# Performance work log

Hardware: AMD Instinct MI355X
Metric: run time of the kernel (lower is better)

The kernel has to match this reference:

```python
import jax, jax.numpy as jnp
import numpy as np

B, S, T = 256, 512, 32  # batch, seq_len, tag_size (includes START=T-2, END=T-1)


def setup_inputs() -> dict:
    key = jax.random.key(0)
    k1, k2, k3, k4 = jax.random.split(key, 4)
    feats = jax.random.normal(k1, (B, S, T), dtype=jnp.float32)
    transitions = jax.random.normal(k2, (T, T), dtype=jnp.float32) * 0.1
    # prefix mask: lengths in [S//2, S] (torch code assumes contiguous valid prefix)
    lengths = jax.random.randint(k3, (B,), S // 2, S + 1)
    mask = jnp.arange(S)[None, :] < lengths[:, None]  # (B,S) bool
    tags = jax.random.randint(k4, (B, S), 0, T - 2).astype(jnp.int32)
    return {"feats": feats, "transitions": transitions, "mask": mask, "tags": tags}


def _nll_loss(feats, transitions, mask, tags):
    Bx, Sx, Tx = feats.shape
    maskf = mask.astype(feats.dtype)
    # ---- forward algorithm (log partition) ----
    # partition initialized from emissions at position 1 (positions 0,1 are special)
    part0 = feats[:, 1, :]  # (B,T)
    f_seq = jnp.swapaxes(feats[:, 2:, :], 0, 1)  # (S-2, B, T)
    m_seq = jnp.swapaxes(mask[:, 2:], 0, 1)      # (S-2, B)

    def fwd_step(partition, inp):
        f_t, m_t = inp
        # cur[b, prev, next] = feats[b,t,next] + transitions[prev,next] + partition[b,prev]
        cur = f_t[:, None, :] + transitions[None, :, :] + partition[:, :, None]
        new = jax.nn.logsumexp(cur, axis=1)  # (B,T)
        # partition frozen where mask==0 (== torch masked_scatter logic)
        return jnp.where(m_t[:, None], new, partition), None

    partition, _ = jax.lax.scan(fwd_step, part0, (f_seq, m_seq))
    forward_score = jnp.sum(jax.nn.logsumexp(partition, axis=1))

    # ---- gold score ----
    tags = jnp.where(tags == -100, 0, tags)
    emis = jnp.take_along_axis(feats, tags[..., None], axis=2)[..., 0]  # (B,S)
    tr = transitions[tags[:, :-1], tags[:, 1:]]  # (B,S-1): transition into pos t (t>=1)
    # transitions only apply for t>=2; tg_energy[0] is zeroed in the torch code
    e = emis + jnp.concatenate([jnp.zeros((Bx, 2), feats.dtype), tr[:, 1:]], axis=1)
    e = e.at[:, 0].set(0.0)
    gold_score = jnp.sum(e * maskf)
    return (forward_score - gold_score) / Bx


def _viterbi(feats, transitions, mask):
    Bx, Sx, Tx = feats.shape
    lengths = mask.astype(jnp.int32).sum(axis=1)
    part0 = feats[:, 1, :]
    f_seq = jnp.swapaxes(feats[:, 2:, :], 0, 1)
    m_seq = jnp.swapaxes(mask[:, 2:], 0, 1)

    def vit_step(partition, inp):
        f_t, m_t = inp
        cur = f_t[:, None, :] + transitions[None, :, :] + partition[:, :, None]
        new = jnp.max(cur, axis=1)
        bp = jnp.argmax(cur, axis=1).astype(jnp.int32)
        bp = jnp.where(m_t[:, None], bp, 0)  # torch masked_fill_(pad, 0)
        # NOTE: viterbi partition is updated UNconditionally in the torch code
        return new, (partition, bp)

    last_part, (hist, bps) = jax.lax.scan(vit_step, part0, (f_seq, m_seq))
    history = jnp.concatenate([hist, last_part[None]], axis=0)  # (S-1,B,T)
    hist_bt = jnp.swapaxes(history, 0, 1)                        # (B,S-1,T)
    idx = jnp.broadcast_to((lengths - 2)[:, None, None], (Bx, 1, Tx))
    last_partition = jnp.take_along_axis(hist_bt, idx, axis=1)[:, 0, :]  # (B,T)
    pointer = jnp.argmax(last_partition, axis=1).astype(jnp.int32)

    def back_step(ptr, bp_t):
        new = jnp.take_along_axis(bp_t, ptr[:, None], axis=1)[:, 0]
        return new, new

    _, ptrs = jax.lax.scan(back_step, pointer, bps, reverse=True)  # (S-2,B)
    # decode_idx[0] is uninitialized in the torch code; we define it as 0
    decode = jnp.concatenate(
        [jnp.zeros((1, Bx), jnp.int32), ptrs, pointer[None, :]], axis=0
    )  # (S,B)
    path_score = jnp.zeros((Bx,), feats.dtype)  # torch returns zeros
    return path_score, decode.T


def reference(feats, transitions, mask, tags):
    loss = _nll_loss(feats, transitions, mask, tags)
    path_score, decode_idx = _viterbi(feats, transitions, mask)
    return loss, path_score, decode_idx
```

## Files before the change

kernel.cpp:

```cpp
#include <hip/hip_runtime.h>
#include <cstdint>
#include <cstddef>
#include <utility>

#define SS 512
#define TT 32
#define NB 256
#define KSTEPS 510
#define PQUADS 128

template <typename F, size_t... Is>
__device__ __forceinline__ void unroll_impl(F&& f, std::index_sequence<Is...>) {
  (f(std::integral_constant<int, (int)Is>{}), ...);
}
template <int N, typename F>
__device__ __forceinline__ void unrollN(F&& f) {
  unroll_impl(f, std::make_index_sequence<N>{});
}

template <int D>
__device__ __forceinline__ float bfly32(float v) {
  return __int_as_float(__builtin_amdgcn_ds_swizzle(__float_as_int(v), (D << 10) | 0x1f));
}
template <int D>
__device__ __forceinline__ int bfly32i(int v) {
  return __builtin_amdgcn_ds_swizzle(v, (D << 10) | 0x1f);
}

__device__ __forceinline__ float max3f(float a, float b, float c) {
  return fmaxf(fmaxf(a, b), c);
}

template <int R>
__device__ __forceinline__ float dpp_rorf(float v) {
  return __int_as_float(__builtin_amdgcn_update_dpp(
      0, __float_as_int(v), 0x120 + R, 0xf, 0xf, true));
}
template <int R>
__device__ __forceinline__ int dpp_rori(int v) {
  return __builtin_amdgcn_update_dpp(0, v, 0x120 + R, 0xf, 0xf, true);
}

__device__ __forceinline__ float combine_max32(float m) {
#if __has_builtin(__builtin_amdgcn_permlane32_swap)
  auto r = __builtin_amdgcn_permlane32_swap(__float_as_uint(m), __float_as_uint(m), false, false);
  return fmaxf(__uint_as_float(r[0]), __uint_as_float(r[1]));
#else
  return fmaxf(m, __shfl_xor(m, 32, 64));
#endif
}
__device__ __forceinline__ float combine_sum32(float m) {
#if __has_builtin(__builtin_amdgcn_permlane32_swap)
  auto r = __builtin_amdgcn_permlane32_swap(__float_as_uint(m), __float_as_uint(m), false, false);
  return __uint_as_float(r[0]) + __uint_as_float(r[1]);
#else
  return m + __shfl_xor(m, 32, 64);
#endif
}
__device__ __forceinline__ float partner16(float v) {
#if __has_builtin(__builtin_amdgcn_permlane16_swap)
  auto r = __builtin_amdgcn_permlane16_swap(__float_as_uint(v), __float_as_uint(v), false, false);
  float a = __uint_as_float(r[0]), b = __uint_as_float(r[1]);
  return (__float_as_uint(a) == __float_as_uint(v)) ? b : a;
#else
  return __shfl_xor(v, 16, 64);
#endif
}

__device__ __forceinline__ int mask_mode(const void* m) {
  int w0 = ((const int*)m)[0];
  if (w0 == 1) return 0;
  if (w0 == 0x3f800000) return 2;
  return 1;
}
__device__ __forceinline__ bool mask_at(const void* m, int idx, int mode) {
  if (mode == 0) return ((const int*)m)[idx] != 0;
  if (mode == 2) return ((const float*)m)[idx] != 0.0f;
  return ((const unsigned char*)m)[idx] != 0;
}

__device__ __forceinline__ int seq_length_lane(const void* mask, int b, int lane, int mode) {
  int cnt = 0;
  for (int s = lane; s < SS; s += 64) cnt += mask_at(mask, b * SS + s, mode) ? 1 : 0;
  for (int d = 1; d < 64; d <<= 1) cnt += __shfl_xor(cnt, d, 64);
  return __builtin_amdgcn_readfirstlane(cnt);
}

__global__ __launch_bounds__(64, 1) void crf_main_kernel(
    const float* __restrict__ feats, const float* __restrict__ trans,
    const void* __restrict__ mask, const int* __restrict__ tags,
    float* __restrict__ pstore, float* __restrict__ ws_fwd,
    float* __restrict__ ws_gold, int* __restrict__ ws_ptr) {
  const int blk = blockIdx.x;
  const int tid = threadIdx.x;
  const int mode = mask_mode(mask);
  const int lane = tid & 63;
  const int l15 = lane & 15;
  const int row = lane >> 4;
  const int heldB = (row == 1 || row == 2) ? 16 : 0;
  const int outB  = (row == 1 || row == 3) ? 16 : 0;
  const int heldtag = l15 + heldB;
  const int outtag  = l15 + outB;
  const bool lower = (lane < 32);

  int src15[16];
  src15[0] = l15;
  unrollN<15>([&](auto RR) { constexpr int r = RR + 1; src15[r] = dpp_rori<r>(l15); });

  if (blk < NB) {
    const int b = blk;
    const int steps = seq_length_lane(mask, b, tid, mode) - 2;
    const float* fb = feats + (size_t)b * (SS * TT) + outtag;

    float E[16];
    unrollN<16>([&](auto RR) {
      constexpr int r = RR;
      E[r] = __expf(trans[(src15[r] + heldB) * TT + outtag]);
    });

    float q = __expf(feats[(size_t)b * (SS * TT) + TT + heldtag]);
    int Eacc = 0;
    float fA = fb[2 * TT], fB = fb[3 * TT], fC = fb[4 * TT];
    float ef = __expf(fA);

    auto fstep = [&](int k, bool resc) {
      int r5 = k + 5; r5 = (r5 < SS) ? r5 : (SS - 1);
      float fD = fb[r5 * TT];
      float efN = __expf(fB);
      float a0 = q * E[0], a1, a2, a3;
      a1 = dpp_rorf<1>(q) * E[1];
      a2 = dpp_rorf<2>(q) * E[2];
      a3 = dpp_rorf<3>(q) * E[3];
      a0 = fmaf(dpp_rorf<4>(q),  E[4],  a0);
      a1 = fmaf(dpp_rorf<5>(q),  E[5],  a1);
      a2 = fmaf(dpp_rorf<6>(q),  E[6],  a2);
      a3 = fmaf(dpp_rorf<7>(q),  E[7],  a3);
      a0 = fmaf(dpp_rorf<8>(q),  E[8],  a0);
      a1 = fmaf(dpp_rorf<9>(q),  E[9],  a1);
      a2 = fmaf(dpp_rorf<10>(q), E[10], a2);
      a3 = fmaf(dpp_rorf<11>(q), E[11], a3);
      a0 = fmaf(dpp_rorf<12>(q), E[12], a0);
      a1 = fmaf(dpp_rorf<13>(q), E[13], a1);
      a2 = fmaf(dpp_rorf<14>(q), E[14], a2);
      a3 = fmaf(dpp_rorf<15>(q), E[15], a3);
      float P = (a0 + a1) + (a2 + a3);
      float val = ef * combine_sum32(P);
      float par = partner16(val);
      float qn = lower ? val : par;
      if (resc) {
        int qb = __builtin_amdgcn_readfirstlane(__float_as_int(qn));
        int e = (qb >> 23) & 0xff;
        Eacc += e - 127;
        qn *= __int_as_float((254 - e) << 23);
      }
      q = qn;
      fA = fB; fB = fC; fC = fD; ef = efN;
    };

    int k = 0;
    for (; k + 4 <= steps; k += 4) {
      fstep(k, false); fstep(k + 1, false); fstep(k + 2, false); fstep(k + 3, true);
    }
    for (; k < steps; ++k) fstep(k, false);

    float s = q;
    unrollN<5>([&](auto D) { constexpr int d = 1 << D; s += bfly32<d>(s); });
    if (tid == 0) ws_fwd[b] = __logf(s) + (float)Eacc * 0.69314718056f;

  } else if (blk < 2 * NB) {
    const int b = blk - NB;
    const int steps = seq_length_lane(mask, b, tid, mode) - 2;
    const float* fb = feats + (size_t)b * (SS * TT) + outtag;
    float* pq = pstore + (size_t)b * (PQUADS * 128) + lane * 4;

    float C[16];
    unrollN<16>([&](auto RR) {
      constexpr int r = RR;
      C[r] = trans[(src15[r] + heldB) * TT + outtag];
    });

    float p = feats[(size_t)b * (SS * TT) + TT + heldtag];
    float fA = fb[2 * TT], fB = fb[3 * TT], fC = fb[4 * TT];
    float h0 = p, h1 = 0.f, h2 = 0.f, h3 = 0.f;

    auto vstep = [&](int k, float& hslot) {
      int r5 = k + 5; r5 = (r5 < SS) ? r5 : (SS - 1);
      float fD = fb[r5 * TT];
      float dd[16];
      unrollN<16>([&](auto RR) { constexpr int r = RR; dd[r] = fA + C[r]; });
      float cur[16];
      cur[0] = p + dd[0];
      cur[1]  = dpp_rorf<1>(p)  + dd[1];
      cur[2]  = dpp_rorf<2>(p)  + dd[2];
      cur[3]  = dpp_rorf<3>(p)  + dd[3];
      cur[4]  = dpp_rorf<4>(p)  + dd[4];
      cur[5]  = dpp_rorf<5>(p)  + dd[5];
      cur[6]  = dpp_rorf<6>(p)  + dd[6];
      cur[7]  = dpp_rorf<7>(p)  + dd[7];
      cur[8]  = dpp_rorf<8>(p)  + dd[8];
      cur[9]  = dpp_rorf<9>(p)  + dd[9];
      cur[10] = dpp_rorf<10>(p) + dd[10];
      cur[11] = dpp_rorf<11>(p) + dd[11];
      cur[12] = dpp_rorf<12>(p) + dd[12];
      cur[13] = dpp_rorf<13>(p) + dd[13];
      cur[14] = dpp_rorf<14>(p) + dd[14];
      cur[15] = dpp_rorf<15>(p) + dd[15];
      float t0 = max3f(cur[0], cur[1], cur[2]);
      float t1 = max3f(cur[3], cur[4], cur[5]);
      float t2 = max3f(cur[6], cur[7], cur[8]);
      float t3 = max3f(cur[9], cur[10], cur[11]);
      float t4 = max3f(cur[12], cur[13], cur[14]);
      float m = fmaxf(max3f(t0, t1, t2), max3f(t3, t4, cur[15]));
      float full = combine_max32(m);
      float par = partner16(full);
      float pw = lower ? full : par;
      p = pw;
      hslot = pw;
      fA = fB; fB = fC; fC = fD;
    };

    auto flush = [&](int quad) {
      if (lane < 32) {
        float4 v; v.x = h0; v.y = h1; v.z = h2; v.w = h3;
        *(float4*)(pq + quad * 128) = v;
      }
    };

    int k = 0;
    for (; k + 4 <= steps; k += 4) {
      vstep(k, h1);
      vstep(k + 1, h2);
      vstep(k + 2, h3);
      flush(k >> 2);
      vstep(k + 3, h0);
    }
    if (k < steps) vstep(k, h1);
    if (k + 1 < steps) vstep(k + 1, h2);
    if (k + 2 < steps) vstep(k + 2, h3);
    flush(k >> 2);

    float v = p;
    int idx = lane & 31;
    unrollN<5>([&](auto D) {
      constexpr int d = 1 << D;
      float vo = bfly32<d>(v);
      int io = bfly32i<d>(idx);
      bool take = (vo > v) || ((vo == v) && (io < idx));
      v = take ? vo : v;
      idx = take ? io : idx;
    });
    if (tid == 0) ws_ptr[b] = idx;

  } else {
    const int b = blk - 2 * NB;
    float acc = 0.0f;
    for (int s = tid; s < SS; s += 64) {
      if (s == 0) continue;
      if (!mask_at(mask, b * SS + s, mode)) continue;
      int tg = tags[b * SS + s];
      if (tg == -100) tg = 0;
      float e = feats[((size_t)b * SS + s) * TT + tg];
      if (s >= 2) {
        int tp = tags[b * SS + s - 1];
        if (tp == -100) tp = 0;
        e += trans[tp * TT + tg];
      }
      acc += e;
    }
    for (int d = 1; d < 64; d <<= 1) acc += __shfl_xor(acc, d, 64);
    if (tid == 0) ws_gold[b] = acc;
  }
}

__global__ __launch_bounds__(512) void crf_backtrace_kernel(
    const float* __restrict__ pstore, const float* __restrict__ feats,
    const float* __restrict__ trans, const void* __restrict__ mask,
    const int* __restrict__ ws_ptr, const float* __restrict__ ws_fwd,
    const float* __restrict__ ws_gold, float* __restrict__ out) {
  __shared__ unsigned char bp[KSTEPS * TT];
  __shared__ unsigned char path[KSTEPS * TT];
  __shared__ __align__(16) float pT[16][4][TT];
  __shared__ int entries[8];

  const int b = blockIdx.x;
  const int tid = threadIdx.x;
  const int mode = mask_mode(mask);
  const int lane = tid & 63;
  float* out_decode = out + 1 + NB;

  const int steps = seq_length_lane(mask, b, lane, mode) - 2;

  if (tid == 0) out[1 + b] = 0.0f;
  if (b == 0 && tid >= 64 && tid < 128) {
    int t = tid - 64;
    float sf = 0.0f, sg = 0.0f;
    for (int r = 0; r < 4; ++r) { sf += ws_fwd[t + 64 * r]; sg += ws_gold[t + 64 * r]; }
    for (int d = 1; d < 64; d <<= 1) { sf += __shfl_xor(sf, d, 64); sg += __shfl_xor(sg, d, 64); }
    if (t == 0) out[0] = (sf - sg) / 256.0f;
  }

  {
    const int jj = tid & 31;
    const int g = tid >> 5;
    float Cc[TT];
    unrollN<TT>([&](auto I) { constexpr int ii = I; Cc[ii] = trans[ii * TT + jj]; });
    const float* pb = pstore + (size_t)b * (PQUADS * 128);
    const float* fbb = feats + (size_t)b * (SS * TT);
    for (int q = g; q < PQUADS; q += 16) {
      float4 V = *(const float4*)(pb + q * 128 + jj * 4);
      pT[g][0][jj] = V.x; pT[g][1][jj] = V.y; pT[g][2][jj] = V.z; pT[g][3][jj] = V.w;
      asm volatile("" ::: "memory");
      unrollN<4>([&](auto R) {
        constexpr int r = R;
        const int k = 4 * q + r;
        if (k < KSTEPS) {
          unsigned char bv = 0;
          if (k < steps) {
            const float4* pr = (const float4*)pT[g][r];
            float4 P0 = pr[0], P1 = pr[1], P2 = pr[2], P3 = pr[3];
            float4 P4 = pr[4], P5 = pr[5], P6 = pr[6], P7 = pr[7];
            float fj = fbb[(k + 2) * TT + jj];
            float cur[TT];
            cur[0]  = (fj + Cc[0])  + P0.x; cur[1]  = (fj + Cc[1])  + P0.y;
            cur[2]  = (fj + Cc[2])  + P0.z; cur[3]  = (fj + Cc[3])  + P0.w;
            cur[4]  = (fj + Cc[4])  + P1.x; cur[5]  = (fj + Cc[5])  + P1.y;
            cur[6]  = (fj + Cc[6])  + P1.z; cur[7]  = (fj + Cc[7])  + P1.w;
            cur[8]  = (fj + Cc[8])  + P2.x; cur[9]  = (fj + Cc[9])  + P2.y;
            cur[10] = (fj + Cc[10]) + P2.z; cur[11] = (fj + Cc[11]) + P2.w;
            cur[12] = (fj + Cc[12]) + P3.x; cur[13] = (fj + Cc[13]) + P3.y;
            cur[14] = (fj + Cc[14]) + P3.z; cur[15] = (fj + Cc[15]) + P3.w;
            cur[16] = (fj + Cc[16]) + P4.x; cur[17] = (fj + Cc[17]) + P4.y;
            cur[18] = (fj + Cc[18]) + P4.z; cur[19] = (fj + Cc[19]) + P4.w;
            cur[20] = (fj + Cc[20]) + P5.x; cur[21] = (fj + Cc[21]) + P5.y;
            cur[22] = (fj + Cc[22]) + P5.z; cur[23] = (fj + Cc[23]) + P5.w;
            cur[24] = (fj + Cc[24]) + P6.x; cur[25] = (fj + Cc[25]) + P6.y;
            cur[26] = (fj + Cc[26]) + P6.z; cur[27] = (fj + Cc[27]) + P6.w;
            cur[28] = (fj + Cc[28]) + P7.x; cur[29] = (fj + Cc[29]) + P7.y;
            cur[30] = (fj + Cc[30]) + P7.z; cur[31] = (fj + Cc[31]) + P7.w;
            float t0 = max3f(cur[0], cur[1], cur[2]);
            float t1 = max3f(cur[3], cur[4], cur[5]);
            float t2 = max3f(cur[6], cur[7], cur[8]);
            float t3 = max3f(cur[9], cur[10], cur[11]);
            float t4 = max3f(cur[12], cur[13], cur[14]);
            float t5 = max3f(cur[15], cur[16], cur[17]);
            float t6 = max3f(cur[18], cur[19], cur[20]);
            float t7 = max3f(cur[21], cur[22], cur[23]);
            float t8 = max3f(cur[24], cur[25], cur[26]);
            float t9 = max3f(cur[27], cur[28], cur[29]);
            float ta = fmaxf(cur[30], cur[31]);
            float vmax = fmaxf(fmaxf(max3f(t0, t1, t2), max3f(t3, t4, t5)),
                               fmaxf(max3f(t6, t7, t8), fmaxf(t9, ta)));
            int bi = 31;
            unrollN<TT>([&](auto I) { constexpr int ii = 31 - I; bi = (cur[ii] == vmax) ? ii : bi; });
            bv = (unsigned char)bi;
          }
          bp[k * TT + jj] = bv;
        }
      });
    }
  }
  __syncthreads();

  const int wave = tid >> 6;
  if (lane < 32) {
    const int lo = wave * 64;
    const int hi = (lo + 64 < KSTEPS) ? (lo + 64) : KSTEPS;
    int ptr = lane;
    for (int k = hi - 1; k >= lo; --k) {
      ptr = bp[k * TT + ptr];
      path[k * TT + lane] = (unsigned char)ptr;
    }
  }
  __syncthreads();

  if (tid == 0) {
    int e = ws_ptr[b];
    for (int c = 7; c >= 0; --c) {
      entries[c] = e;
      e = path[(c * 64) * TT + e];
    }
  }
  __syncthreads();

  const int s = tid;
  int val;
  if (s == 0) val = 0;
  else if (s <= KSTEPS) { int k = s - 1; val = path[k * TT + entries[k >> 6]]; }
  else val = ws_ptr[b];
  out_decode[(size_t)b * SS + s] = (float)val;
}

extern "C" void kernel_launch(void* const* d_in, const int* in_sizes, int n_in,
                              void* d_out, int out_size, void* d_ws, size_t ws_size,
                              hipStream_t stream) {
  const float* feats = (const float*)d_in[0];
  const float* trans = (const float*)d_in[1];
  const void* mask = d_in[2];
  const int* tags = (const int*)d_in[3];
  float* out = (float*)d_out;

  unsigned char* ws = (unsigned char*)d_ws;
  const size_t PST_BYTES = (size_t)NB * PQUADS * 128 * 4;
  float* pstore = (float*)ws;
  float* ws_fwd = (float*)(ws + PST_BYTES);
  float* ws_gold = (float*)(ws + PST_BYTES + 2048);
  int* ws_ptr = (int*)(ws + PST_BYTES + 4096);

  hipLaunchKernelGGL(crf_main_kernel, dim3(3 * NB), dim3(64), 0, stream,
                     feats, trans, mask, tags, pstore, ws_fwd, ws_gold, ws_ptr);
  hipLaunchKernelGGL(crf_backtrace_kernel, dim3(NB), dim3(512), 0, stream,
                     pstore, feats, trans, mask, ws_ptr, ws_fwd, ws_gold, out);
}
```

Before: 103.6 us.

## Transpose feats to tag-major layout so recurrences load float4 rows

Adds a pre-pass kernel that transposes feats from (B,S,T) to (B,T,S) in workspace. The forward and Viterbi recurrences then read four timesteps per lane with one float4 load instead of one strided scalar load per step, which is meant to cut latency-bound memory traffic in the serial loop. The new path is used only when the workspace is large enough, with the old kernel kept as a fallback. It costs an extra launch and a full read and write of feats (about 16 MB each way).

After: 113.5 us. 1.1x slower.

```diff
diff --git a/kernel.cpp b/kernel.cpp
--- a/kernel.cpp
+++ b/kernel.cpp
@@ -86,7 +86,227 @@
   return __builtin_amdgcn_readfirstlane(cnt);
 }
 
-__global__ __launch_bounds__(64, 1) void crf_main_kernel(
+__global__ __launch_bounds__(256) void crf_transpose_kernel(
+    const float* __restrict__ feats, float* __restrict__ ftr) {
+  const int b = blockIdx.x;
+  const int tid = threadIdx.x;
+  __shared__ float tile[TT][72];
+
+  for (int tile0 = 0; tile0 < SS; tile0 += 64) {
+    for (int i = tid; i < 512; i += 256) {
+      int s_local = i >> 3, g = i & 7;
+      float4 v = *(const float4*)(feats + ((size_t)(b * SS + tile0 + s_local)) * TT + 4 * g);
+      tile[4 * g + 0][s_local] = v.x;
+      tile[4 * g + 1][s_local] = v.y;
+      tile[4 * g + 2][s_local] = v.z;
+      tile[4 * g + 3][s_local] = v.w;
+    }
+    __syncthreads();
+    {
+      int t = tid >> 3, sc = tid & 7;
+      float4 a, c;
+      a.x = tile[t][sc * 8 + 0]; a.y = tile[t][sc * 8 + 1];
+      a.z = tile[t][sc * 8 + 2]; a.w = tile[t][sc * 8 + 3];
+      c.x = tile[t][sc * 8 + 4]; c.y = tile[t][sc * 8 + 5];
+      c.z = tile[t][sc * 8 + 6]; c.w = tile[t][sc * 8 + 7];
+      float* dst = ftr + ((size_t)(b * TT + t)) * SS + tile0 + sc * 8;
+      *(float4*)dst = a;
+      *(float4*)(dst + 4) = c;
+    }
+    __syncthreads();
+  }
+}
+
+__global__ __launch_bounds__(64, 1) void crf_main_kernel_t(
+    const float* __restrict__ feats, const float* __restrict__ ftr,
+    const float* __restrict__ trans, const void* __restrict__ mask,
+    const int* __restrict__ tags, float* __restrict__ pstore,
+    float* __restrict__ ws_fwd, float* __restrict__ ws_gold,
+    int* __restrict__ ws_ptr) {
+  const int blk = blockIdx.x;
+  const int tid = threadIdx.x;
+  const int mode = mask_mode(mask);
+  const int lane = tid & 63;
+  const int l15 = lane & 15;
+  const int row = lane >> 4;
+  const int heldB = (row == 1 || row == 2) ? 16 : 0;
+  const int outB  = (row == 1 || row == 3) ? 16 : 0;
+  const int heldtag = l15 + heldB;
+  const int outtag  = l15 + outB;
+  const bool lower = (lane < 32);
+
+  int src15[16];
+  src15[0] = l15;
+  unrollN<15>([&](auto RR) { constexpr int r = RR + 1; src15[r] = dpp_rori<r>(l15); });
+
+  if (blk < NB) {
+    const int b = blk;
+    const int steps = seq_length_lane(mask, b, tid, mode) - 2;
+    const float* fr = ftr + ((size_t)(b * TT + outtag)) * SS;
+
+    float E[16];
+    unrollN<16>([&](auto RR) {
+      constexpr int r = RR;
+      E[r] = __expf(trans[(src15[r] + heldB) * TT + outtag]);
+    });
+
+    float q = __expf(ftr[((size_t)(b * TT + heldtag)) * SS + 1]);
+    int Eacc = 0;
+
+    auto fstep = [&](float ef, bool resc) {
+      float a0 = q * E[0], a1, a2, a3;
+      a1 = dpp_rorf<1>(q) * E[1];
+      a2 = dpp_rorf<2>(q) * E[2];
+      a3 = dpp_rorf<3>(q) * E[3];
+      a0 = fmaf(dpp_rorf<4>(q),  E[4],  a0);
+      a1 = fmaf(dpp_rorf<5>(q),  E[5],  a1);
+      a2 = fmaf(dpp_rorf<6>(q),  E[6],  a2);
+      a3 = fmaf(dpp_rorf<7>(q),  E[7],  a3);
+      a0 = fmaf(dpp_rorf<8>(q),  E[8],  a0);
+      a1 = fmaf(dpp_rorf<9>(q),  E[9],  a1);
+      a2 = fmaf(dpp_rorf<10>(q), E[10], a2);
+      a3 = fmaf(dpp_rorf<11>(q), E[11], a3);
+      a0 = fmaf(dpp_rorf<12>(q), E[12], a0);
+      a1 = fmaf(dpp_rorf<13>(q), E[13], a1);
+      a2 = fmaf(dpp_rorf<14>(q), E[14], a2);
+      a3 = fmaf(dpp_rorf<15>(q), E[15], a3);
+      float P = (a0 + a1) + (a2 + a3);
+      float val = ef * combine_sum32(P);
+      float par = partner16(val);
+      float qn = lower ? val : par;
+      if (resc) {
+        int qb = __builtin_amdgcn_readfirstlane(__float_as_int(qn));
+        int e = (qb >> 23) & 0xff;
+        Eacc += e - 127;
+        qn *= __int_as_float((254 - e) << 23);
+      }
+      q = qn;
+    };
+
+    float4 R0 = *(const float4*)(fr + 0), R1 = *(const float4*)(fr + 4);
+    float4 R2 = *(const float4*)(fr + 8), R3 = *(const float4*)(fr + 12);
+    int qd = 0;
+    for (; 4 * qd + 4 <= steps; ++qd) {
+      int mq = qd + 4; mq = (mq < 127) ? mq : 127;
+      float4 Rn = *(const float4*)(fr + 4 * mq);
+      float e0 = __expf(R0.z), e1 = __expf(R0.w), e2 = __expf(R1.x), e3 = __expf(R1.y);
+      fstep(e0, false); fstep(e1, false); fstep(e2, false); fstep(e3, true);
+      R0 = R1; R1 = R2; R2 = R3; R3 = Rn;
+    }
+    for (int k = 4 * qd; k < steps; ++k) fstep(__expf(fr[k + 2]), false);
+
+    float s = q;
+    unrollN<5>([&](auto D) { constexpr int d = 1 << D; s += bfly32<d>(s); });
+    if (tid == 0) ws_fwd[b] = __logf(s) + (float)Eacc * 0.69314718056f;
+
+  } else if (blk < 2 * NB) {
+    const int b = blk - NB;
+    const int steps = seq_length_lane(mask, b, tid, mode) - 2;
+    const float* fr = ftr + ((size_t)(b * TT + outtag)) * SS;
+    float* pq = pstore + (size_t)b * (PQUADS * 128) + lane * 4;
+
+    float C[16];
+    unrollN<16>([&](auto RR) {
+      constexpr int r = RR;
+      C[r] = trans[(src15[r] + heldB) * TT + outtag];
+    });
+
+    float p = ftr[((size_t)(b * TT + heldtag)) * SS + 1];
+    float h0 = p, h1 = 0.f, h2 = 0.f, h3 = 0.f;
+
+    auto vstep = [&](float f, float& hslot) {
+      float dd[16];
+      unrollN<16>([&](auto RR) { constexpr int r = RR; dd[r] = f + C[r]; });
+      float cur[16];
+      cur[0] = p + dd[0];
+      cur[1]  = dpp_rorf<1>(p)  + dd[1];
+      cur[2]  = dpp_rorf<2>(p)  + dd[2];
+      cur[3]  = dpp_rorf<3>(p)  + dd[3];
+      cur[4]  = dpp_rorf<4>(p)  + dd[4];
+      cur[5]  = dpp_rorf<5>(p)  + dd[5];
+      cur[6]  = dpp_rorf<6>(p)  + dd[6];
+      cur[7]  = dpp_rorf<7>(p)  + dd[7];
+      cur[8]  = dpp_rorf<8>(p)  + dd[8];
+      cur[9]  = dpp_rorf<9>(p)  + dd[9];
+      cur[10] = dpp_rorf<10>(p) + dd[10];
+      cur[11] = dpp_rorf<11>(p) + dd[11];
+      cur[12] = dpp_rorf<12>(p) + dd[12];
+      cur[13] = dpp_rorf<13>(p) + dd[13];
+      cur[14] = dpp_rorf<14>(p) + dd[14];
+      cur[15] = dpp_rorf<15>(p) + dd[15];
+      float t0 = max3f(cur[0], cur[1], cur[2]);
+      float t1 = max3f(cur[3], cur[4], cur[5]);
+      float t2 = max3f(cur[6], cur[7], cur[8]);
+      float t3 = max3f(cur[9], cur[10], cur[11]);
+      float t4 = max3f(cur[12], cur[13], cur[14]);
+      float m = fmaxf(max3f(t0, t1, t2), max3f(t3, t4, cur[15]));
+      float full = combine_max32(m);
+      float par = partner16(full);
+      float pw = lower ? full : par;
+      p = pw;
+      hslot = pw;
+    };
+
+    auto flush = [&](int quad) {
+      if (lane < 32) {
+        float4 v; v.x = h0; v.y = h1; v.z = h2; v.w = h3;
+        *(float4*)(pq + quad * 128) = v;
+      }
+    };
+
+    float4 R0 = *(const float4*)(fr + 0), R1 = *(const float4*)(fr + 4);
+    float4 R2 = *(const float4*)(fr + 8), R3 = *(const float4*)(fr + 12);
+    int qd = 0;
+    for (; 4 * qd + 4 <= steps; ++qd) {
+      int mq = qd + 4; mq = (mq < 127) ? mq : 127;
+      float4 Rn = *(const float4*)(fr + 4 * mq);
+      vstep(R0.z, h1);
+      vstep(R0.w, h2);
+      vstep(R1.x, h3);
+      flush(qd);
+      vstep(R1.y, h0);
+      R0 = R1; R1 = R2; R2 = R3; R3 = Rn;
+    }
+    int k = 4 * qd;
+    if (k < steps) vstep(fr[k + 2], h1);
+    if (k + 1 < steps) vstep(fr[k + 3], h2);
+    if (k + 2 < steps) vstep(fr[k + 4], h3);
+    flush(qd);
+
+    float v = p;
+    int idx = lane & 31;
+    unrollN<5>([&](auto D) {
+      constexpr int d = 1 << D;
+      float vo = bfly32<d>(v);
+      int io = bfly32i<d>(idx);
+      bool take = (vo > v) || ((vo == v) && (io < idx));
+      v = take ? vo : v;
+      idx = take ? io : idx;
+    });
+    if (tid == 0) ws_ptr[b] = idx;
+
+  } else {
+    const int b = blk - 2 * NB;
+    float acc = 0.0f;
+    for (int s = tid; s < SS; s += 64) {
+      if (s == 0) continue;
+      if (!mask_at(mask, b * SS + s, mode)) continue;
+      int tg = tags[b * SS + s];
+      if (tg == -100) tg = 0;
+      float e = feats[((size_t)b * SS + s) * TT + tg];
+      if (s >= 2) {
+        int tp = tags[b * SS + s - 1];
+        if (tp == -100) tp = 0;
+        e += trans[tp * TT + tg];
+      }
+      acc += e;
+    }
+    for (int d = 1; d < 64; d <<= 1) acc += __shfl_xor(acc, d, 64);
+    if (tid == 0) ws_gold[b] = acc;
+  }
+}
+
+__global__ __launch_bounds__(64, 1) void crf_main_kernel_legacy(
     const float* __restrict__ feats, const float* __restrict__ trans,
     const void* __restrict__ mask, const int* __restrict__ tags,
     float* __restrict__ pstore, float* __restrict__ ws_fwd,
@@ -111,18 +331,15 @@
     const int b = blk;
     const int steps = seq_length_lane(mask, b, tid, mode) - 2;
     const float* fb = feats + (size_t)b * (SS * TT) + outtag;
-
     float E[16];
     unrollN<16>([&](auto RR) {
       constexpr int r = RR;
       E[r] = __expf(trans[(src15[r] + heldB) * TT + outtag]);
     });
-
     float q = __expf(feats[(size_t)b * (SS * TT) + TT + heldtag]);
     int Eacc = 0;
     float fA = fb[2 * TT], fB = fb[3 * TT], fC = fb[4 * TT];
     float ef = __expf(fA);
-
     auto fstep = [&](int k, bool resc) {
       int r5 = k + 5; r5 = (r5 < SS) ? r5 : (SS - 1);
       float fD = fb[r5 * TT];
@@ -156,13 +373,11 @@
       q = qn;
       fA = fB; fB = fC; fC = fD; ef = efN;
     };
-
     int k = 0;
     for (; k + 4 <= steps; k += 4) {
       fstep(k, false); fstep(k + 1, false); fstep(k + 2, false); fstep(k + 3, true);
     }
     for (; k < steps; ++k) fstep(k, false);
-
     float s = q;
     unrollN<5>([&](auto D) { constexpr int d = 1 << D; s += bfly32<d>(s); });
     if (tid == 0) ws_fwd[b] = __logf(s) + (float)Eacc * 0.69314718056f;
@@ -172,17 +387,14 @@
     const int steps = seq_length_lane(mask, b, tid, mode) - 2;
     const float* fb = feats + (size_t)b * (SS * TT) + outtag;
     float* pq = pstore + (size_t)b * (PQUADS * 128) + lane * 4;
-
     float C[16];
     unrollN<16>([&](auto RR) {
       constexpr int r = RR;
       C[r] = trans[(src15[r] + heldB) * TT + outtag];
     });
-
     float p = feats[(size_t)b * (SS * TT) + TT + heldtag];
     float fA = fb[2 * TT], fB = fb[3 * TT], fC = fb[4 * TT];
     float h0 = p, h1 = 0.f, h2 = 0.f, h3 = 0.f;
-
     auto vstep = [&](int k, float& hslot) {
       int r5 = k + 5; r5 = (r5 < SS) ? r5 : (SS - 1);
       float fD = fb[r5 * TT];
@@ -218,19 +430,15 @@
       hslot = pw;
       fA = fB; fB = fC; fC = fD;
     };
-
     auto flush = [&](int quad) {
       if (lane < 32) {
         float4 v; v.x = h0; v.y = h1; v.z = h2; v.w = h3;
         *(float4*)(pq + quad * 128) = v;
       }
     };
-
     int k = 0;
     for (; k + 4 <= steps; k += 4) {
-      vstep(k, h1);
-      vstep(k + 1, h2);
-      vstep(k + 2, h3);
+      vstep(k, h1); vstep(k + 1, h2); vstep(k + 2, h3);
       flush(k >> 2);
       vstep(k + 3, h0);
     }
@@ -238,7 +446,6 @@
     if (k + 1 < steps) vstep(k + 1, h2);
     if (k + 2 < steps) vstep(k + 2, h3);
     flush(k >> 2);
-
     float v = p;
     int idx = lane & 31;
     unrollN<5>([&](auto D) {
@@ -401,13 +608,25 @@
 
   unsigned char* ws = (unsigned char*)d_ws;
   const size_t PST_BYTES = (size_t)NB * PQUADS * 128 * 4;
+  const size_t FTR_BYTES = (size_t)NB * TT * SS * 4;
+  const bool useT = (ws_size >= PST_BYTES + FTR_BYTES + 8192);
+
   float* pstore = (float*)ws;
-  float* ws_fwd = (float*)(ws + PST_BYTES);
-  float* ws_gold = (float*)(ws + PST_BYTES + 2048);
-  int* ws_ptr = (int*)(ws + PST_BYTES + 4096);
-
-  hipLaunchKernelGGL(crf_main_kernel, dim3(3 * NB), dim3(64), 0, stream,
-                     feats, trans, mask, tags, pstore, ws_fwd, ws_gold, ws_ptr);
+  float* ftr = (float*)(ws + PST_BYTES);
+  const size_t small_off = useT ? (PST_BYTES + FTR_BYTES) : PST_BYTES;
+  float* ws_fwd = (float*)(ws + small_off);
+  float* ws_gold = (float*)(ws + small_off + 2048);
+  int* ws_ptr = (int*)(ws + small_off + 4096);
+
+  if (useT) {
+    hipLaunchKernelGGL(crf_transpose_kernel, dim3(NB), dim3(256), 0, stream,
+                       feats, ftr);
+    hipLaunchKernelGGL(crf_main_kernel_t, dim3(3 * NB), dim3(64), 0, stream,
+                       feats, ftr, trans, mask, tags, pstore, ws_fwd, ws_gold, ws_ptr);
+  } else {
+    hipLaunchKernelGGL(crf_main_kernel_legacy, dim3(3 * NB), dim3(64), 0, stream,
+                       feats, trans, mask, tags, pstore, ws_fwd, ws_gold, ws_ptr);
+  }
   hipLaunchKernelGGL(crf_backtrace_kernel, dim3(NB), dim3(512), 0, stream,
                      pstore, feats, trans, mask, ws_ptr, ws_fwd, ws_gold, out);
 }
```

## Split backpointer recomputation into a separate widely-parallel kernel before backtrace

Applied to the files above, without the earlier changes.

When the workspace is large enough, backpointer recomputation moves out of the per-batch 512-thread backtrace kernel into its own kernel with 16 blocks per batch element. That kernel writes byte backpointers to global workspace, and a lighter backtrace kernel copies them into shared memory and follows the pointer chains. The aim is more parallelism and occupancy for the compute-heavy argmax step. The cost is an extra kernel launch plus a global write and read of about 4 MB of backpointers. If the workspace is too small, the original single backtrace kernel runs instead.

Measured after the change: 109.4 us. 1.06x slower.

```diff
diff --git a/kernel.cpp b/kernel.cpp
--- a/kernel.cpp
+++ b/kernel.cpp
@@ -111,18 +111,15 @@
     const int b = blk;
     const int steps = seq_length_lane(mask, b, tid, mode) - 2;
     const float* fb = feats + (size_t)b * (SS * TT) + outtag;
-
     float E[16];
     unrollN<16>([&](auto RR) {
       constexpr int r = RR;
       E[r] = __expf(trans[(src15[r] + heldB) * TT + outtag]);
     });
-
     float q = __expf(feats[(size_t)b * (SS * TT) + TT + heldtag]);
     int Eacc = 0;
     float fA = fb[2 * TT], fB = fb[3 * TT], fC = fb[4 * TT];
     float ef = __expf(fA);
-
     auto fstep = [&](int k, bool resc) {
       int r5 = k + 5; r5 = (r5 < SS) ? r5 : (SS - 1);
       float fD = fb[r5 * TT];
@@ -156,13 +153,11 @@
       q = qn;
       fA = fB; fB = fC; fC = fD; ef = efN;
     };
-
     int k = 0;
     for (; k + 4 <= steps; k += 4) {
       fstep(k, false); fstep(k + 1, false); fstep(k + 2, false); fstep(k + 3, true);
     }
     for (; k < steps; ++k) fstep(k, false);
-
     float s = q;
     unrollN<5>([&](auto D) { constexpr int d = 1 << D; s += bfly32<d>(s); });
     if (tid == 0) ws_fwd[b] = __logf(s) + (float)Eacc * 0.69314718056f;
@@ -172,17 +167,14 @@
     const int steps = seq_length_lane(mask, b, tid, mode) - 2;
     const float* fb = feats + (size_t)b * (SS * TT) + outtag;
     float* pq = pstore + (size_t)b * (PQUADS * 128) + lane * 4;
-
     float C[16];
     unrollN<16>([&](auto RR) {
       constexpr int r = RR;
       C[r] = trans[(src15[r] + heldB) * TT + outtag];
     });
-
     float p = feats[(size_t)b * (SS * TT) + TT + heldtag];
     float fA = fb[2 * TT], fB = fb[3 * TT], fC = fb[4 * TT];
     float h0 = p, h1 = 0.f, h2 = 0.f, h3 = 0.f;
-
     auto vstep = [&](int k, float& hslot) {
       int r5 = k + 5; r5 = (r5 < SS) ? r5 : (SS - 1);
       float fD = fb[r5 * TT];
@@ -218,19 +210,15 @@
       hslot = pw;
       fA = fB; fB = fC; fC = fD;
     };
-
     auto flush = [&](int quad) {
       if (lane < 32) {
         float4 v; v.x = h0; v.y = h1; v.z = h2; v.w = h3;
         *(float4*)(pq + quad * 128) = v;
       }
     };
-
     int k = 0;
     for (; k + 4 <= steps; k += 4) {
-      vstep(k, h1);
-      vstep(k + 1, h2);
-      vstep(k + 2, h3);
+      vstep(k, h1); vstep(k + 1, h2); vstep(k + 2, h3);
       flush(k >> 2);
       vstep(k + 3, h0);
     }
@@ -238,7 +226,6 @@
     if (k + 1 < steps) vstep(k + 1, h2);
     if (k + 2 < steps) vstep(k + 2, h3);
     flush(k >> 2);
-
     float v = p;
     int idx = lane & 31;
     unrollN<5>([&](auto D) {
@@ -270,6 +257,138 @@
     for (int d = 1; d < 64; d <<= 1) acc += __shfl_xor(acc, d, 64);
     if (tid == 0) ws_gold[b] = acc;
   }
+}
+
+__device__ __forceinline__ unsigned char bp_compute(
+    const float* pr , float fj, const float (&Cc)[TT]) {
+  const float4* p4 = (const float4*)pr;
+  float4 P0 = p4[0], P1 = p4[1], P2 = p4[2], P3 = p4[3];
+  float4 P4 = p4[4], P5 = p4[5], P6 = p4[6], P7 = p4[7];
+  float cur[TT];
+  cur[0]  = (fj + Cc[0])  + P0.x; cur[1]  = (fj + Cc[1])  + P0.y;
+  cur[2]  = (fj + Cc[2])  + P0.z; cur[3]  = (fj + Cc[3])  + P0.w;
+  cur[4]  = (fj + Cc[4])  + P1.x; cur[5]  = (fj + Cc[5])  + P1.y;
+  cur[6]  = (fj + Cc[6])  + P1.z; cur[7]  = (fj + Cc[7])  + P1.w;
+  cur[8]  = (fj + Cc[8])  + P2.x; cur[9]  = (fj + Cc[9])  + P2.y;
+  cur[10] = (fj + Cc[10]) + P2.z; cur[11] = (fj + Cc[11]) + P2.w;
+  cur[12] = (fj + Cc[12]) + P3.x; cur[13] = (fj + Cc[13]) + P3.y;
+  cur[14] = (fj + Cc[14]) + P3.z; cur[15] = (fj + Cc[15]) + P3.w;
+  cur[16] = (fj + Cc[16]) + P4.x; cur[17] = (fj + Cc[17]) + P4.y;
+  cur[18] = (fj + Cc[18]) + P4.z; cur[19] = (fj + Cc[19]) + P4.w;
+  cur[20] = (fj + Cc[20]) + P5.x; cur[21] = (fj + Cc[21]) + P5.y;
+  cur[22] = (fj + Cc[22]) + P5.z; cur[23] = (fj + Cc[23]) + P5.w;
+  cur[24] = (fj + Cc[24]) + P6.x; cur[25] = (fj + Cc[25]) + P6.y;
+  cur[26] = (fj + Cc[26]) + P6.z; cur[27] = (fj + Cc[27]) + P6.w;
+  cur[28] = (fj + Cc[28]) + P7.x; cur[29] = (fj + Cc[29]) + P7.y;
+  cur[30] = (fj + Cc[30]) + P7.z; cur[31] = (fj + Cc[31]) + P7.w;
+  float t0 = max3f(cur[0], cur[1], cur[2]);
+  float t1 = max3f(cur[3], cur[4], cur[5]);
+  float t2 = max3f(cur[6], cur[7], cur[8]);
+  float t3 = max3f(cur[9], cur[10], cur[11]);
+  float t4 = max3f(cur[12], cur[13], cur[14]);
+  float t5 = max3f(cur[15], cur[16], cur[17]);
+  float t6 = max3f(cur[18], cur[19], cur[20]);
+  float t7 = max3f(cur[21], cur[22], cur[23]);
+  float t8 = max3f(cur[24], cur[25], cur[26]);
+  float t9 = max3f(cur[27], cur[28], cur[29]);
+  float ta = fmaxf(cur[30], cur[31]);
+  float vmax = fmaxf(fmaxf(max3f(t0, t1, t2), max3f(t3, t4, t5)),
+                     fmaxf(max3f(t6, t7, t8), fmaxf(t9, ta)));
+  int bi = 31;
+  unrollN<TT>([&](auto I) { constexpr int ii = 31 - I; bi = (cur[ii] == vmax) ? ii : bi; });
+  return (unsigned char)bi;
+}
+
+__global__ __launch_bounds__(256) void crf_bp_kernel(
+    const float* __restrict__ pstore, const float* __restrict__ feats,
+    const float* __restrict__ trans, const void* __restrict__ mask,
+    unsigned char* __restrict__ ws_bp) {
+  const int bid = blockIdx.x;
+  const int b = bid >> 4;
+  const int qg = bid & 15;
+  const int tid = threadIdx.x;
+  const int jj = tid & 31;
+  const int g = tid >> 5;
+  const int q = qg * 8 + g;
+  const int mode = mask_mode(mask);
+  const int steps = seq_length_lane(mask, b, tid & 63, mode) - 2;
+
+  __shared__ __align__(16) float pT[8][4][TT];
+
+  float Cc[TT];
+  unrollN<TT>([&](auto I) { constexpr int ii = I; Cc[ii] = trans[ii * TT + jj]; });
+  const float* pb = pstore + (size_t)b * (PQUADS * 128);
+  const float* fbb = feats + (size_t)b * (SS * TT);
+  unsigned char* bpb = ws_bp + (size_t)b * (KSTEPS * TT);
+
+  float4 V = *(const float4*)(pb + q * 128 + jj * 4);
+  pT[g][0][jj] = V.x; pT[g][1][jj] = V.y; pT[g][2][jj] = V.z; pT[g][3][jj] = V.w;
+  asm volatile("" ::: "memory");
+  unrollN<4>([&](auto R) {
+    constexpr int r = R;
+    const int k = 4 * q + r;
+    if (k < KSTEPS) {
+      unsigned char bv = 0;
+      if (k < steps) bv = bp_compute(pT[g][r], fbb[(k + 2) * TT + jj], Cc);
+      bpb[k * TT + jj] = bv;
+    }
+  });
+}
+
+__global__ __launch_bounds__(512) void crf_backtrace2_kernel(
+    const unsigned char* __restrict__ ws_bp, const int* __restrict__ ws_ptr,
+    const float* __restrict__ ws_fwd, const float* __restrict__ ws_gold,
+    float* __restrict__ out) {
+  __shared__ unsigned char bp[KSTEPS * TT];
+  __shared__ unsigned char path[KSTEPS * TT];
+  __shared__ int entries[8];
+
+  const int b = blockIdx.x;
+  const int tid = threadIdx.x;
+  float* out_decode = out + 1 + NB;
+
+  if (tid == 0) out[1 + b] = 0.0f;
+  if (b == 0 && tid >= 64 && tid < 128) {
+    int t = tid - 64;
+    float sf = 0.0f, sg = 0.0f;
+    for (int r = 0; r < 4; ++r) { sf += ws_fwd[t + 64 * r]; sg += ws_gold[t + 64 * r]; }
+    for (int d = 1; d < 64; d <<= 1) { sf += __shfl_xor(sf, d, 64); sg += __shfl_xor(sg, d, 64); }
+    if (t == 0) out[0] = (sf - sg) / 256.0f;
+  }
+
+  const int* src = (const int*)(ws_bp + (size_t)b * (KSTEPS * TT));
+  int* dst = (int*)bp;
+  for (int w = tid; w < KSTEPS * 8; w += 512) dst[w] = src[w];
+  __syncthreads();
+
+  const int wave = tid >> 6;
+  const int lane = tid & 63;
+  if (lane < 32) {
+    const int lo = wave * 64;
+    const int hi = (lo + 64 < KSTEPS) ? (lo + 64) : KSTEPS;
+    int ptr = lane;
+    for (int k = hi - 1; k >= lo; --k) {
+      ptr = bp[k * TT + ptr];
+      path[k * TT + lane] = (unsigned char)ptr;
+    }
+  }
+  __syncthreads();
+
+  if (tid == 0) {
+    int e = ws_ptr[b];
+    for (int c = 7; c >= 0; --c) {
+      entries[c] = e;
+      e = path[(c * 64) * TT + e];
+    }
+  }
+  __syncthreads();
+
+  const int s = tid;
+  int val;
+  if (s == 0) val = 0;
+  else if (s <= KSTEPS) { int k = s - 1; val = path[k * TT + entries[k >> 6]]; }
+  else val = ws_ptr[b];
+  out_decode[(size_t)b * SS + s] = (float)val;
 }
 
 __global__ __launch_bounds__(512) void crf_backtrace_kernel(
@@ -315,45 +434,7 @@
         const int k = 4 * q + r;
         if (k < KSTEPS) {
           unsigned char bv = 0;
-          if (k < steps) {
-            const float4* pr = (const float4*)pT[g][r];
-            float4 P0 = pr[0], P1 = pr[1], P2 = pr[2], P3 = pr[3];
-            float4 P4 = pr[4], P5 = pr[5], P6 = pr[6], P7 = pr[7];
-            float fj = fbb[(k + 2) * TT + jj];
-            float cur[TT];
-            cur[0]  = (fj + Cc[0])  + P0.x; cur[1]  = (fj + Cc[1])  + P0.y;
-            cur[2]  = (fj + Cc[2])  + P0.z; cur[3]  = (fj + Cc[3])  + P0.w;
-            cur[4]  = (fj + Cc[4])  + P1.x; cur[5]  = (fj + Cc[5])  + P1.y;
-            cur[6]  = (fj + Cc[6])  + P1.z; cur[7]  = (fj + Cc[7])  + P1.w;
-            cur[8]  = (fj + Cc[8])  + P2.x; cur[9]  = (fj + Cc[9])  + P2.y;
-            cur[10] = (fj + Cc[10]) + P2.z; cur[11] = (fj + Cc[11]) + P2.w;
-            cur[12] = (fj + Cc[12]) + P3.x; cur[13] = (fj + Cc[13]) + P3.y;
-            cur[14] = (fj + Cc[14]) + P3.z; cur[15] = (fj + Cc[15]) + P3.w;
-            cur[16] = (fj + Cc[16]) + P4.x; cur[17] = (fj + Cc[17]) + P4.y;
-            cur[18] = (fj + Cc[18]) + P4.z; cur[19] = (fj + Cc[19]) + P4.w;
-            cur[20] = (fj + Cc[20]) + P5.x; cur[21] = (fj + Cc[21]) + P5.y;
-            cur[22] = (fj + Cc[22]) + P5.z; cur[23] = (fj + Cc[23]) + P5.w;
-            cur[24] = (fj + Cc[24]) + P6.x; cur[25] = (fj + Cc[25]) + P6.y;
-            cur[26] = (fj + Cc[26]) + P6.z; cur[27] = (fj + Cc[27]) + P6.w;
-            cur[28] = (fj + Cc[28]) + P7.x; cur[29] = (fj + Cc[29]) + P7.y;
-            cur[30] = (fj + Cc[30]) + P7.z; cur[31] = (fj + Cc[31]) + P7.w;
-            float t0 = max3f(cur[0], cur[1], cur[2]);
-            float t1 = max3f(cur[3], cur[4], cur[5]);
-            float t2 = max3f(cur[6], cur[7], cur[8]);
-            float t3 = max3f(cur[9], cur[10], cur[11]);
-            float t4 = max3f(cur[12], cur[13], cur[14]);
-            float t5 = max3f(cur[15], cur[16], cur[17]);
-            float t6 = max3f(cur[18], cur[19], cur[20]);
-            float t7 = max3f(cur[21], cur[22], cur[23]);
-            float t8 = max3f(cur[24], cur[25], cur[26]);
-            float t9 = max3f(cur[27], cur[28], cur[29]);
-            float ta = fmaxf(cur[30], cur[31]);
-            float vmax = fmaxf(fmaxf(max3f(t0, t1, t2), max3f(t3, t4, t5)),
-                               fmaxf(max3f(t6, t7, t8), fmaxf(t9, ta)));
-            int bi = 31;
-            unrollN<TT>([&](auto I) { constexpr int ii = 31 - I; bi = (cur[ii] == vmax) ? ii : bi; });
-            bv = (unsigned char)bi;
-          }
+          if (k < steps) bv = bp_compute(pT[g][r], fbb[(k + 2) * TT + jj], Cc);
           bp[k * TT + jj] = bv;
         }
       });
@@ -401,13 +482,25 @@
 
   unsigned char* ws = (unsigned char*)d_ws;
   const size_t PST_BYTES = (size_t)NB * PQUADS * 128 * 4;
+  const size_t BP_BYTES = ((size_t)NB * KSTEPS * TT + 4095) & ~(size_t)4095;
+  const bool split = (ws_size >= PST_BYTES + BP_BYTES + 8192);
+
   float* pstore = (float*)ws;
-  float* ws_fwd = (float*)(ws + PST_BYTES);
-  float* ws_gold = (float*)(ws + PST_BYTES + 2048);
-  int* ws_ptr = (int*)(ws + PST_BYTES + 4096);
+  unsigned char* ws_bp = ws + PST_BYTES;
+  const size_t small_off = split ? (PST_BYTES + BP_BYTES) : PST_BYTES;
+  float* ws_fwd = (float*)(ws + small_off);
+  float* ws_gold = (float*)(ws + small_off + 2048);
+  int* ws_ptr = (int*)(ws + small_off + 4096);
 
   hipLaunchKernelGGL(crf_main_kernel, dim3(3 * NB), dim3(64), 0, stream,
                      feats, trans, mask, tags, pstore, ws_fwd, ws_gold, ws_ptr);
-  hipLaunchKernelGGL(crf_backtrace_kernel, dim3(NB), dim3(512), 0, stream,
-                     pstore, feats, trans, mask, ws_ptr, ws_fwd, ws_gold, out);
-}
+  if (split) {
+    hipLaunchKernelGGL(crf_bp_kernel, dim3(NB * 16), dim3(256), 0, stream,
+                       pstore, feats, trans, mask, ws_bp);
+    hipLaunchKernelGGL(crf_backtrace2_kernel, dim3(NB), dim3(512), 0, stream,
+                       ws_bp, ws_ptr, ws_fwd, ws_gold, out);
+  } else {
+    hipLaunchKernelGGL(crf_backtrace_kernel, dim3(NB), dim3(512), 0, stream,
+                       pstore, feats, trans, mask, ws_ptr, ws_fwd, ws_gold, out);
+  }
+}
```

## Compute Viterbi backpointers inline in forward pass instead of recomputing in backtrace

Applied to the files above, without the earlier changes.

The Viterbi wave now derives the argmax backpointer at every step from a bitmask of equality matches, combined across lane halves with ctz, and writes one byte per tag to workspace. Before, it stored the full partition history and the backtrace kernel recomputed all 32x32 max and argmax values. The backtrace kernel now only copies the byte backpointers into LDS. This removes a large recomputation and cuts workspace traffic, at the cost of extra ALU and cross-lane work on the serial Viterbi critical path.

Result: slower. 157.5 us (+52.0%).

```diff
diff --git a/kernel.cpp b/kernel.cpp
--- a/kernel.cpp
+++ b/kernel.cpp
@@ -7,7 +7,6 @@
 #define TT 32
 #define NB 256
 #define KSTEPS 510
-#define PQUADS 128
 
 template <typename F, size_t... Is>
 __device__ __forceinline__ void unroll_impl(F&& f, std::index_sequence<Is...>) {
@@ -55,6 +54,15 @@
   return __uint_as_float(r[0]) + __uint_as_float(r[1]);
 #else
   return m + __shfl_xor(m, 32, 64);
+#endif
+}
+__device__ __forceinline__ int partner32i(int v) {
+#if __has_builtin(__builtin_amdgcn_permlane32_swap)
+  auto r = __builtin_amdgcn_permlane32_swap((unsigned)v, (unsigned)v, false, false);
+  int a = (int)r[0], b = (int)r[1];
+  return (a == v) ? b : a;
+#else
+  return __shfl_xor(v, 32, 64);
 #endif
 }
 __device__ __forceinline__ float partner16(float v) {
@@ -89,7 +97,7 @@
 __global__ __launch_bounds__(64, 1) void crf_main_kernel(
     const float* __restrict__ feats, const float* __restrict__ trans,
     const void* __restrict__ mask, const int* __restrict__ tags,
-    float* __restrict__ pstore, float* __restrict__ ws_fwd,
+    unsigned char* __restrict__ ws_bp, float* __restrict__ ws_fwd,
     float* __restrict__ ws_gold, int* __restrict__ ws_ptr) {
   const int blk = blockIdx.x;
   const int tid = threadIdx.x;
@@ -102,6 +110,7 @@
   const int heldtag = l15 + heldB;
   const int outtag  = l15 + outB;
   const bool lower = (lane < 32);
+  const bool isLow = (heldB == 0);
 
   int src15[16];
   src15[0] = l15;
@@ -111,18 +120,15 @@
     const int b = blk;
     const int steps = seq_length_lane(mask, b, tid, mode) - 2;
     const float* fb = feats + (size_t)b * (SS * TT) + outtag;
-
     float E[16];
     unrollN<16>([&](auto RR) {
       constexpr int r = RR;
       E[r] = __expf(trans[(src15[r] + heldB) * TT + outtag]);
     });
-
     float q = __expf(feats[(size_t)b * (SS * TT) + TT + heldtag]);
     int Eacc = 0;
     float fA = fb[2 * TT], fB = fb[3 * TT], fC = fb[4 * TT];
     float ef = __expf(fA);
-
     auto fstep = [&](int k, bool resc) {
       int r5 = k + 5; r5 = (r5 < SS) ? r5 : (SS - 1);
       float fD = fb[r5 * TT];
@@ -156,13 +162,11 @@
       q = qn;
       fA = fB; fB = fC; fC = fD; ef = efN;
     };
-
     int k = 0;
     for (; k + 4 <= steps; k += 4) {
       fstep(k, false); fstep(k + 1, false); fstep(k + 2, false); fstep(k + 3, true);
     }
     for (; k < steps; ++k) fstep(k, false);
-
     float s = q;
     unrollN<5>([&](auto D) { constexpr int d = 1 << D; s += bfly32<d>(s); });
     if (tid == 0) ws_fwd[b] = __logf(s) + (float)Eacc * 0.69314718056f;
@@ -171,19 +175,20 @@
     const int b = blk - NB;
     const int steps = seq_length_lane(mask, b, tid, mode) - 2;
     const float* fb = feats + (size_t)b * (SS * TT) + outtag;
-    float* pq = pstore + (size_t)b * (PQUADS * 128) + lane * 4;
+    unsigned char* bpb = ws_bp + (size_t)b * (KSTEPS * TT) + outtag;
 
     float C[16];
+    int bitpos[16];
     unrollN<16>([&](auto RR) {
       constexpr int r = RR;
       C[r] = trans[(src15[r] + heldB) * TT + outtag];
+      bitpos[r] = 1 << src15[r];
     });
 
     float p = feats[(size_t)b * (SS * TT) + TT + heldtag];
     float fA = fb[2 * TT], fB = fb[3 * TT], fC = fb[4 * TT];
-    float h0 = p, h1 = 0.f, h2 = 0.f, h3 = 0.f;
-
-    auto vstep = [&](int k, float& hslot) {
+
+    auto vstep = [&](int k) {
       int r5 = k + 5; r5 = (r5 < SS) ? r5 : (SS - 1);
       float fD = fb[r5 * TT];
       float dd[16];
@@ -211,33 +216,27 @@
       float t3 = max3f(cur[9], cur[10], cur[11]);
       float t4 = max3f(cur[12], cur[13], cur[14]);
       float m = fmaxf(max3f(t0, t1, t2), max3f(t3, t4, cur[15]));
-      float full = combine_max32(m);
-      float par = partner16(full);
-      float pw = lower ? full : par;
+      float vmax = combine_max32(m);
+      float par = partner16(vmax);
+      float pw = lower ? vmax : par;
       p = pw;
-      hslot = pw;
+      int msk = 0;
+      unrollN<16>([&](auto RR) {
+        constexpr int r = RR;
+        msk |= (cur[r] == vmax) ? bitpos[r] : 0;
+      });
+      int pmsk = partner32i(msk);
+      int lowM = isLow ? msk : pmsk;
+      int highM = isLow ? pmsk : msk;
+      int mask32 = lowM | (highM << 16);
+      int bi = __builtin_ctz(mask32);
+      if (lower) bpb[k * TT] = (unsigned char)bi;
       fA = fB; fB = fC; fC = fD;
     };
 
-    auto flush = [&](int quad) {
-      if (lane < 32) {
-        float4 v; v.x = h0; v.y = h1; v.z = h2; v.w = h3;
-        *(float4*)(pq + quad * 128) = v;
-      }
-    };
-
     int k = 0;
-    for (; k + 4 <= steps; k += 4) {
-      vstep(k, h1);
-      vstep(k + 1, h2);
-      vstep(k + 2, h3);
-      flush(k >> 2);
-      vstep(k + 3, h0);
-    }
-    if (k < steps) vstep(k, h1);
-    if (k + 1 < steps) vstep(k + 1, h2);
-    if (k + 2 < steps) vstep(k + 2, h3);
-    flush(k >> 2);
+    for (; k + 4 <= steps; k += 4) { vstep(k); vstep(k + 1); vstep(k + 2); vstep(k + 3); }
+    for (; k < steps; ++k) vstep(k);
 
     float v = p;
     int idx = lane & 31;
@@ -250,6 +249,9 @@
       idx = take ? io : idx;
     });
     if (tid == 0) ws_ptr[b] = idx;
+
+    int* bpw = (int*)(ws_bp + (size_t)b * (KSTEPS * TT));
+    for (int w = steps * 8 + tid; w < KSTEPS * 8; w += 64) bpw[w] = 0;
 
   } else {
     const int b = blk - 2 * NB;
@@ -273,22 +275,16 @@
 }
 
 __global__ __launch_bounds__(512) void crf_backtrace_kernel(
-    const float* __restrict__ pstore, const float* __restrict__ feats,
-    const float* __restrict__ trans, const void* __restrict__ mask,
-    const int* __restrict__ ws_ptr, const float* __restrict__ ws_fwd,
-    const float* __restrict__ ws_gold, float* __restrict__ out) {
+    const unsigned char* __restrict__ ws_bp, const int* __restrict__ ws_ptr,
+    const float* __restrict__ ws_fwd, const float* __restrict__ ws_gold,
+    float* __restrict__ out) {
   __shared__ unsigned char bp[KSTEPS * TT];
   __shared__ unsigned char path[KSTEPS * TT];
-  __shared__ __align__(16) float pT[16][4][TT];
   __shared__ int entries[8];
 
   const int b = blockIdx.x;
   const int tid = threadIdx.x;
-  const int mode = mask_mode(mask);
-  const int lane = tid & 63;
   float* out_decode = out + 1 + NB;
-
-  const int steps = seq_length_lane(mask, b, lane, mode) - 2;
 
   if (tid == 0) out[1 + b] = 0.0f;
   if (b == 0 && tid >= 64 && tid < 128) {
@@ -299,69 +295,13 @@
     if (t == 0) out[0] = (sf - sg) / 256.0f;
   }
 
-  {
-    const int jj = tid & 31;
-    const int g = tid >> 5;
-    float Cc[TT];
-    unrollN<TT>([&](auto I) { constexpr int ii = I; Cc[ii] = trans[ii * TT + jj]; });
-    const float* pb = pstore + (size_t)b * (PQUADS * 128);
-    const float* fbb = feats + (size_t)b * (SS * TT);
-    for (int q = g; q < PQUADS; q += 16) {
-      float4 V = *(const float4*)(pb + q * 128 + jj * 4);
-      pT[g][0][jj] = V.x; pT[g][1][jj] = V.y; pT[g][2][jj] = V.z; pT[g][3][jj] = V.w;
-      asm volatile("" ::: "memory");
-      unrollN<4>([&](auto R) {
-        constexpr int r = R;
-        const int k = 4 * q + r;
-        if (k < KSTEPS) {
-          unsigned char bv = 0;
-          if (k < steps) {
-            const float4* pr = (const float4*)pT[g][r];
-            float4 P0 = pr[0], P1 = pr[1], P2 = pr[2], P3 = pr[3];
-            float4 P4 = pr[4], P5 = pr[5], P6 = pr[6], P7 = pr[7];
-            float fj = fbb[(k + 2) * TT + jj];
-            float cur[TT];
-            cur[0]  = (fj + Cc[0])  + P0.x; cur[1]  = (fj + Cc[1])  + P0.y;
-            cur[2]  = (fj + Cc[2])  + P0.z; cur[3]  = (fj + Cc[3])  + P0.w;
-            cur[4]  = (fj + Cc[4])  + P1.x; cur[5]  = (fj + Cc[5])  + P1.y;
-            cur[6]  = (fj + Cc[6])  + P1.z; cur[7]  = (fj + Cc[7])  + P1.w;
-            cur[8]  = (fj + Cc[8])  + P2.x; cur[9]  = (fj + Cc[9])  + P2.y;
-            cur[10] = (fj + Cc[10]) + P2.z; cur[11] = (fj + Cc[11]) + P2.w;
-            cur[12] = (fj + Cc[12]) + P3.x; cur[13] = (fj + Cc[13]) + P3.y;
-            cur[14] = (fj + Cc[14]) + P3.z; cur[15] = (fj + Cc[15]) + P3.w;
-            cur[16] = (fj + Cc[16]) + P4.x; cur[17] = (fj + Cc[17]) + P4.y;
-            cur[18] = (fj + Cc[18]) + P4.z; cur[19] = (fj + Cc[19]) + P4.w;
-            cur[20] = (fj + Cc[20]) + P5.x; cur[21] = (fj + Cc[21]) + P5.y;
-            cur[22] = (fj + Cc[22]) + P5.z; cur[23] = (fj + Cc[23]) + P5.w;
-            cur[24] = (fj + Cc[24]) + P6.x; cur[25] = (fj + Cc[25]) + P6.y;
-            cur[26] = (fj + Cc[26]) + P6.z; cur[27] = (fj + Cc[27]) + P6.w;
-            cur[28] = (fj + Cc[28]) + P7.x; cur[29] = (fj + Cc[29]) + P7.y;
-            cur[30] = (fj + Cc[30]) + P7.z; cur[31] = (fj + Cc[31]) + P7.w;
-            float t0 = max3f(cur[0], cur[1], cur[2]);
-            float t1 = max3f(cur[3], cur[4], cur[5]);
-            float t2 = max3f(cur[6], cur[7], cur[8]);
-            float t3 = max3f(cur[9], cur[10], cur[11]);
-            float t4 = max3f(cur[12], cur[13], cur[14]);
-            float t5 = max3f(cur[15], cur[16], cur[17]);
-            float t6 = max3f(cur[18], cur[19], cur[20]);
-            float t7 = max3f(cur[21], cur[22], cur[23]);
-            float t8 = max3f(cur[24], cur[25], cur[26]);
-            float t9 = max3f(cur[27], cur[28], cur[29]);
-            float ta = fmaxf(cur[30], cur[31]);
-            float vmax = fmaxf(fmaxf(max3f(t0, t1, t2), max3f(t3, t4, t5)),
-                               fmaxf(max3f(t6, t7, t8), fmaxf(t9, ta)));
-            int bi = 31;
-            unrollN<TT>([&](auto I) { constexpr int ii = 31 - I; bi = (cur[ii] == vmax) ? ii : bi; });
-            bv = (unsigned char)bi;
-          }
-          bp[k * TT + jj] = bv;
-        }
-      });
-    }
-  }
+  const int* src = (const int*)(ws_bp + (size_t)b * (KSTEPS * TT));
+  int* dst = (int*)bp;
+  for (int w = tid; w < KSTEPS * 8; w += 512) dst[w] = src[w];
   __syncthreads();
 
   const int wave = tid >> 6;
+  const int lane = tid & 63;
   if (lane < 32) {
     const int lo = wave * 64;
     const int hi = (lo + 64 < KSTEPS) ? (lo + 64) : KSTEPS;
@@ -400,14 +340,14 @@
   float* out = (float*)d_out;
 
   unsigned char* ws = (unsigned char*)d_ws;
-  const size_t PST_BYTES = (size_t)NB * PQUADS * 128 * 4;
-  float* pstore = (float*)ws;
-  float* ws_fwd = (float*)(ws + PST_BYTES);
-  float* ws_gold = (float*)(ws + PST_BYTES + 2048);
-  int* ws_ptr = (int*)(ws + PST_BYTES + 4096);
+  const size_t BP_BYTES = (size_t)NB * KSTEPS * TT;
+  unsigned char* ws_bp = ws;
+  float* ws_fwd = (float*)(ws + BP_BYTES + 128);
+  float* ws_gold = (float*)(ws + BP_BYTES + 2048 + 128);
+  int* ws_ptr = (int*)(ws + BP_BYTES + 4096 + 128);
 
   hipLaunchKernelGGL(crf_main_kernel, dim3(3 * NB), dim3(64), 0, stream,
-                     feats, trans, mask, tags, pstore, ws_fwd, ws_gold, ws_ptr);
+                     feats, trans, mask, tags, ws_bp, ws_fwd, ws_gold, ws_ptr);
   hipLaunchKernelGGL(crf_backtrace_kernel, dim3(NB), dim3(512), 0, stream,
-                     pstore, feats, trans, mask, ws_ptr, ws_fwd, ws_gold, out);
-}
+                     ws_bp, ws_ptr, ws_fwd, ws_gold, out);
+}
```
